# Kernel tuning notes

Hardware: AMD Instinct MI355X
Metric: run time of the kernel (lower is better)

The kernel has to match this reference:

```python
import jax, jax.numpy as jnp
import numpy as np

B = 131072   # batch of state samples
H = 512      # hidden width of reconstructed subnets
EPS_DIAG = 0.1  # diagonal regularization ensuring M is invertible


def setup_inputs() -> dict:
    key = jax.random.key(0)
    ks = jax.random.split(key, 20)
    f32 = jnp.float32
    inp = {
        "q":      jax.random.normal(ks[0], (B, 3), dtype=f32),
        "q_dot":  jax.random.normal(ks[1], (B, 3), dtype=f32),
        "s":      jax.random.normal(ks[2], (B, 3), dtype=f32),
        "s_Ddot": jax.random.normal(ks[3], (B, 3), dtype=f32),
        "tau":    jax.random.normal(ks[4], (B, 3), dtype=f32),
        # viscous / coulomb friction coefficients (f_v1..3, f_c1..3)
        "fv": jnp.full((3,), 0.05, dtype=f32),
        "fc": jnp.full((3,), 0.05, dtype=f32),
        # Mass net: 3 -> H -> 9
        "W1m": jax.random.normal(ks[5], (3, H), dtype=f32) * 0.1,
        "b1m": jnp.zeros((H,), dtype=f32),
        "W2m": jax.random.normal(ks[6], (H, 9), dtype=f32) * 0.05,
        "b2m": jnp.zeros((9,), dtype=f32),
        # Gravity net: 3 -> H -> 3
        "W1g": jax.random.normal(ks[7], (3, H), dtype=f32) * 0.1,
        "b1g": jnp.zeros((H,), dtype=f32),
        "W2g": jax.random.normal(ks[8], (H, 3), dtype=f32) * 0.05,
        "b2g": jnp.zeros((3,), dtype=f32),
        # KAB net: concat(q, s, s_Ddot)=9 -> H -> 3
        "W1k": jax.random.normal(ks[9], (9, H), dtype=f32) * 0.1,
        "b1k": jnp.zeros((H,), dtype=f32),
        "W2k": jax.random.normal(ks[10], (H, 3), dtype=f32) * 0.05,
        "b2k": jnp.zeros((3,), dtype=f32),
    }
    return inp


def reference(q, q_dot, s, s_Ddot, tau, fv, fc,
              W1m, b1m, W2m, b2m,
              W1g, b1g, W2g, b2g,
              W1k, b1k, W2k, b2k) -> jnp.ndarray:
    # Mass matrix net -> [B,3,3], made SPD-ish so inv(M) is well defined
    hm = jnp.tanh(q @ W1m + b1m)                       # [B,H]
    Mraw = (hm @ W2m + b2m).reshape(-1, 3, 3)          # [B,3,3]
    M = jnp.einsum('bij,bkj->bik', Mraw, Mraw) + EPS_DIAG * jnp.eye(3, dtype=q.dtype)

    # Gravity net -> [B,3]
    hg = jnp.tanh(q @ W1g + b1g)
    G = hg @ W2g + b2g

    # KAB net on concat(q, s, s_Ddot) -> [B,3]
    x = jnp.concatenate([q, s, s_Ddot], axis=-1)       # [B,9]
    hk = jnp.tanh(x @ W1k + b1k)
    KAB = hk @ W2k + b2k

    # diag(fv) @ q_dot and diag(fc) @ sign(q_dot) are elementwise scalings
    rhs = -G + KAB - fv * q_dot - fc * jnp.sign(q_dot) + tau  # [B,3]

    # q_Ddot = inv(M) @ rhs  (solve is the same math, fewer ops)
    q_Ddot = jnp.linalg.solve(M, rhs[..., None]).squeeze(-1)  # [B,3]
    return q_Ddot
```

## Files before the change

kernel.cpp:

```cpp
#include <hip/hip_runtime.h>
#include <math.h>

#define HDIM 512
#define NCH1 96
#define NCH2 48
#define EPS_DIAG 0.1f

typedef __fp16 h2 __attribute__((ext_vector_type(2)));
typedef __fp16 h8 __attribute__((ext_vector_type(8)));
typedef float f32x4 __attribute__((ext_vector_type(4)));
typedef unsigned int u32x4 __attribute__((ext_vector_type(4)));

__device__ __forceinline__ h2 f2h2(float a, float b) {
    return __builtin_amdgcn_cvt_pkrtz(a, b);
}

__device__ __forceinline__ h2 tanh2(h2 x) {
    const h2 HI = {(__fp16)2.0f,        (__fp16)2.0f};
    const h2 LO = {(__fp16)-2.0f,       (__fp16)-2.0f};
    const h2 C0 = {(__fp16)0.993654f,   (__fp16)0.993654f};
    const h2 C1 = {(__fp16)-0.29463f,   (__fp16)-0.29463f};
    const h2 C2 = {(__fp16)0.0695331f,  (__fp16)0.0695331f};
    const h2 C3 = {(__fp16)-0.00696328f,(__fp16)-0.00696328f};
    h2 t = __builtin_elementwise_min(__builtin_elementwise_max(x, LO), HI);
    h2 u = t * t;
    h2 p = __builtin_elementwise_fma(C3, u, C2);
    p = __builtin_elementwise_fma(p, u, C1);
    p = __builtin_elementwise_fma(p, u, C0);
    return t * p;
}

__device__ __forceinline__ float w1c_at(int k, int hid,
    const float* W1m, const float* b1m, const float* W1g, const float* b1g,
    const float* W1k, const float* b1k)
{
    if (hid < 512)  { if (k < 3) return W1m[k*HDIM + hid]; if (k == 9) return b1m[hid]; return 0.f; }
    if (hid < 1024) { const int h = hid - 512;
                      if (k < 3) return W1g[k*HDIM + h];  if (k == 9) return b1g[h];  return 0.f; }
    const int h = hid - 1024;
    if (k < 9) return W1k[k*HDIM + h]; if (k == 9) return b1k[h]; return 0.f;
}

__global__ void pack_frags(const float* __restrict__ W1m, const float* __restrict__ b1m,
                           const float* __restrict__ W2m,
                           const float* __restrict__ W1g, const float* __restrict__ b1g,
                           const float* __restrict__ W2g,
                           const float* __restrict__ W1k, const float* __restrict__ b1k,
                           const float* __restrict__ W2k,
                           __fp16* __restrict__ frag)
{
    const int tid = blockIdx.x * blockDim.x + threadIdx.x;
    if (tid >= (NCH1 + NCH2) * 64) return;
    const int c = tid >> 6, l = tid & 63;
    const int m = l & 15, kq = l >> 4;
    __fp16* dst = frag + (size_t)tid * 8;
    if (c < NCH1) {
        const int t = c >> 1, phase = c & 1;
        const int hid = 32*t + 8*(m >> 2) + (m & 3) + 4*phase;
        #pragma unroll
        for (int j = 0; j < 8; ++j) {
            const int k = kq*8 + j;
            dst[j] = (__fp16)((k < 10) ? w1c_at(k, hid, W1m, b1m, W1g, b1g, W1k, b1k) : 0.f);
        }
    } else {
        const int t = c - NCH1;
        #pragma unroll
        for (int j = 0; j < 8; ++j) {
            const int hid = 32*t + kq*8 + j;
            float v = 0.f;
            if (hid < 512)       { if (m < 9)             v = W2m[hid*9 + m]; }
            else if (hid < 1024) { if (m >= 9 && m < 12)  v = W2g[(hid-512)*3 + (m-9)]; }
            else                 { if (m >= 12 && m < 15) v = W2k[(hid-1024)*3 + (m-12)]; }
            dst[j] = (__fp16)v;
        }
    }
}

__global__ __launch_bounds__(256, 8) void dyn_kernel(
    const __fp16* __restrict__ frag,
    const float* __restrict__ q, const float* __restrict__ q_dot,
    const float* __restrict__ s, const float* __restrict__ s_Ddot,
    const float* __restrict__ tau,
    const float* __restrict__ fv, const float* __restrict__ fc,
    const float* __restrict__ b2m, const float* __restrict__ b2g,
    const float* __restrict__ b2k,
    float* __restrict__ out, int n)
{
    __shared__ float ebuf[4][16][20];

    const int lane = threadIdx.x & 63;
    const int w    = threadIdx.x >> 6;
    const int col  = lane & 15;
    const int quad = lane >> 4;
    const int base16 = (blockIdx.x * 4 + w) * 16;

    int sm = base16 + col; if (sm >= n) sm = n - 1;
    const float q0 = q[3*sm+0], q1 = q[3*sm+1], q2 = q[3*sm+2];
    const float s0 = s[3*sm+0], s1 = s[3*sm+1], s2 = s[3*sm+2];
    const float d0 = s_Ddot[3*sm+0], d1 = s_Ddot[3*sm+1], d2 = s_Ddot[3*sm+2];
    const bool z0 = (quad == 0), z1 = (quad == 1);
    h8 ax;
    ax[0] = (__fp16)(z0 ? q0 : (z1 ? d2  : 0.f));
    ax[1] = (__fp16)(z0 ? q1 : (z1 ? 1.f : 0.f));
    ax[2] = (__fp16)(z0 ? q2 : 0.f);
    ax[3] = (__fp16)(z0 ? s0 : 0.f);
    ax[4] = (__fp16)(z0 ? s1 : 0.f);
    ax[5] = (__fp16)(z0 ? s2 : 0.f);
    ax[6] = (__fp16)(z0 ? d0 : 0.f);
    ax[7] = (__fp16)(z0 ? d1 : 0.f);

    const f32x4 zero4 = {0.f, 0.f, 0.f, 0.f};
    f32x4 acc = zero4;

    const h8* p1 = (const h8*)frag + lane;
    const h8* p2 = (const h8*)frag + (size_t)NCH1 * 64 + lane;

#define BODY(W1A, W1B, W2V) do {                                              \
        f32x4 pa = __builtin_amdgcn_mfma_f32_16x16x32_f16((W1A), ax, zero4, 0, 0, 0); \
        f32x4 pb = __builtin_amdgcn_mfma_f32_16x16x32_f16((W1B), ax, zero4, 0, 0, 0); \
        const h2 A01 = tanh2(f2h2(pa[0], pa[1]));                             \
        const h2 A23 = tanh2(f2h2(pa[2], pa[3]));                             \
        const h2 B01 = tanh2(f2h2(pb[0], pb[1]));                             \
        const h2 B23 = tanh2(f2h2(pb[2], pb[3]));                             \
        u32x4 uv;                                                             \
        uv[0] = __builtin_bit_cast(unsigned int, A01);                        \
        uv[1] = __builtin_bit_cast(unsigned int, A23);                        \
        uv[2] = __builtin_bit_cast(unsigned int, B01);                        \
        uv[3] = __builtin_bit_cast(unsigned int, B23);                        \
        const h8 a2 = __builtin_bit_cast(h8, uv);                             \
        acc = __builtin_amdgcn_mfma_f32_16x16x32_f16((W2V), a2, acc, 0, 0, 0); \
    } while (0)

    h8 a0 = p1[0], b0 = p1[64], c0 = p2[0];
    int t = 0;
    for (; t < NCH2 - 2; t += 2) {
        h8 a1 = p1[128], b1 = p1[192], c1 = p2[64];
        p1 += 256; p2 += 128;
        BODY(a0, b0, c0);
        a0 = p1[0]; b0 = p1[64]; c0 = p2[0];
        BODY(a1, b1, c1);
    }
    {
        h8 a1 = p1[128], b1 = p1[192], c1 = p2[64];
        BODY(a0, b0, c0);
        BODY(a1, b1, c1);
    }
#undef BODY

    *(f32x4*)(&ebuf[w][col][4*quad]) = acc;
    asm volatile("s_waitcnt lgkmcnt(0)" ::: "memory");

    if (lane < 16) {
        const int i = base16 + lane;
        if (i < n) {
            const float* R = ebuf[w][lane];
            const float bM0 = R[0]  + b2m[0], bM1 = R[1]  + b2m[1], bM2 = R[2]  + b2m[2];
            const float bM3 = R[3]  + b2m[3], bM4 = R[4]  + b2m[4], bM5 = R[5]  + b2m[5];
            const float bM6 = R[6]  + b2m[6], bM7 = R[7]  + b2m[7], bM8 = R[8]  + b2m[8];
            const float bG0 = R[9]  + b2g[0], bG1 = R[10] + b2g[1], bG2 = R[11] + b2g[2];
            const float bK0 = R[12] + b2k[0], bK1 = R[13] + b2k[1], bK2 = R[14] + b2k[2];

            const float m00 = bM0*bM0 + bM1*bM1 + bM2*bM2 + EPS_DIAG;
            const float m01 = bM0*bM3 + bM1*bM4 + bM2*bM5;
            const float m02 = bM0*bM6 + bM1*bM7 + bM2*bM8;
            const float m11 = bM3*bM3 + bM4*bM4 + bM5*bM5 + EPS_DIAG;
            const float m12 = bM3*bM6 + bM4*bM7 + bM5*bM8;
            const float m22 = bM6*bM6 + bM7*bM7 + bM8*bM8 + EPS_DIAG;

            const float qd0 = q_dot[3*i+0], qd1 = q_dot[3*i+1], qd2 = q_dot[3*i+2];
            const float t0 = tau[3*i+0], t1 = tau[3*i+1], t2 = tau[3*i+2];
            const float fv0 = fv[0], fv1 = fv[1], fv2 = fv[2];
            const float fc0 = fc[0], fc1 = fc[1], fc2 = fc[2];
            const float sg0 = (qd0 > 0.f) ? 1.f : ((qd0 < 0.f) ? -1.f : 0.f);
            const float sg1 = (qd1 > 0.f) ? 1.f : ((qd1 < 0.f) ? -1.f : 0.f);
            const float sg2 = (qd2 > 0.f) ? 1.f : ((qd2 < 0.f) ? -1.f : 0.f);
            const float r0 = -bG0 + bK0 - fv0*qd0 - fc0*sg0 + t0;
            const float r1 = -bG1 + bK1 - fv1*qd1 - fc1*sg1 + t1;
            const float r2 = -bG2 + bK2 - fv2*qd2 - fc2*sg2 + t2;

            const float c00 = m11*m22 - m12*m12;
            const float c01 = m02*m12 - m01*m22;
            const float c02 = m01*m12 - m02*m11;
            const float det = m00*c00 + m01*c01 + m02*c02;
            const float idet = 1.0f / det;
            const float i11 = m00*m22 - m02*m02;
            const float i12 = m01*m02 - m00*m12;
            const float i22 = m00*m11 - m01*m01;

            out[3*i+0] = (c00*r0 + c01*r1 + c02*r2) * idet;
            out[3*i+1] = (c01*r0 + i11*r1 + i12*r2) * idet;
            out[3*i+2] = (c02*r0 + i12*r1 + i22*r2) * idet;
        }
    }
}

extern "C" void kernel_launch(void* const* d_in, const int* in_sizes, int n_in,
                              void* d_out, int out_size, void* d_ws, size_t ws_size,
                              hipStream_t stream) {
    const float* q      = (const float*)d_in[0];
    const float* q_dot  = (const float*)d_in[1];
    const float* s      = (const float*)d_in[2];
    const float* s_Ddot = (const float*)d_in[3];
    const float* tau    = (const float*)d_in[4];
    const float* fv     = (const float*)d_in[5];
    const float* fc     = (const float*)d_in[6];
    const float* W1m    = (const float*)d_in[7];
    const float* b1m    = (const float*)d_in[8];
    const float* W2m    = (const float*)d_in[9];
    const float* b2m    = (const float*)d_in[10];
    const float* W1g    = (const float*)d_in[11];
    const float* b1g    = (const float*)d_in[12];
    const float* W2g    = (const float*)d_in[13];
    const float* b2g    = (const float*)d_in[14];
    const float* W1k    = (const float*)d_in[15];
    const float* b1k    = (const float*)d_in[16];
    const float* W2k    = (const float*)d_in[17];
    const float* b2k    = (const float*)d_in[18];
    float* out = (float*)d_out;
    __fp16* frag = (__fp16*)d_ws;

    const int n = in_sizes[0] / 3;

    pack_frags<<<((NCH1 + NCH2) * 64 + 255) / 256, 256, 0, stream>>>(
        W1m, b1m, W2m, W1g, b1g, W2g, W1k, b1k, W2k, frag);

    const int blocks = (n + 63) / 64;
    dyn_kernel<<<blocks, 256, 0, stream>>>(frag, q, q_dot, s, s_Ddot, tau, fv, fc,
                                           b2m, b2g, b2k, out, n);
}
```

Baseline: 133.7 us.

## Process two 16-sample tiles per wave to reuse weight fragments

Each wave now handles 32 samples instead of 16, running two sets of MFMAs against each loaded weight fragment. This halves global/L2 weight fragment traffic per sample and halves the grid size, giving more independent MFMA work per loaded fragment. Launch bounds occupancy hint drops from 8 to 4 to allow more registers for the doubled accumulators and activations, which lowers occupancy. The epilogue now uses 32 lanes per wave for the solve.

```diff
diff --git a/kernel.cpp b/kernel.cpp
--- a/kernel.cpp
+++ b/kernel.cpp
@@ -76,7 +76,7 @@
     }
 }
 
-__global__ __launch_bounds__(256, 8) void dyn_kernel(
+__global__ __launch_bounds__(256, 4) void dyn_kernel(
     const __fp16* __restrict__ frag,
     const float* __restrict__ q, const float* __restrict__ q_dot,
     const float* __restrict__ s, const float* __restrict__ s_Ddot,
@@ -86,49 +86,68 @@
     const float* __restrict__ b2k,
     float* __restrict__ out, int n)
 {
-    __shared__ float ebuf[4][16][20];
+    __shared__ float ebuf[4][32][20];
 
     const int lane = threadIdx.x & 63;
     const int w    = threadIdx.x >> 6;
     const int col  = lane & 15;
     const int quad = lane >> 4;
-    const int base16 = (blockIdx.x * 4 + w) * 16;
-
-    int sm = base16 + col; if (sm >= n) sm = n - 1;
-    const float q0 = q[3*sm+0], q1 = q[3*sm+1], q2 = q[3*sm+2];
-    const float s0 = s[3*sm+0], s1 = s[3*sm+1], s2 = s[3*sm+2];
-    const float d0 = s_Ddot[3*sm+0], d1 = s_Ddot[3*sm+1], d2 = s_Ddot[3*sm+2];
-    const bool z0 = (quad == 0), z1 = (quad == 1);
-    h8 ax;
-    ax[0] = (__fp16)(z0 ? q0 : (z1 ? d2  : 0.f));
-    ax[1] = (__fp16)(z0 ? q1 : (z1 ? 1.f : 0.f));
-    ax[2] = (__fp16)(z0 ? q2 : 0.f);
-    ax[3] = (__fp16)(z0 ? s0 : 0.f);
-    ax[4] = (__fp16)(z0 ? s1 : 0.f);
-    ax[5] = (__fp16)(z0 ? s2 : 0.f);
-    ax[6] = (__fp16)(z0 ? d0 : 0.f);
-    ax[7] = (__fp16)(z0 ? d1 : 0.f);
+    const int base32 = (blockIdx.x * 4 + w) * 32;
+
+    h8 ax0, ax1;
+    {
+        int sm = base32 + col; if (sm >= n) sm = n - 1;
+        const float q0 = q[3*sm+0], q1 = q[3*sm+1], q2 = q[3*sm+2];
+        const float s0 = s[3*sm+0], s1 = s[3*sm+1], s2 = s[3*sm+2];
+        const float d0 = s_Ddot[3*sm+0], d1 = s_Ddot[3*sm+1], d2 = s_Ddot[3*sm+2];
+        const bool z0 = (quad == 0), z1 = (quad == 1);
+        ax0[0] = (__fp16)(z0 ? q0 : (z1 ? d2  : 0.f));
+        ax0[1] = (__fp16)(z0 ? q1 : (z1 ? 1.f : 0.f));
+        ax0[2] = (__fp16)(z0 ? q2 : 0.f);
+        ax0[3] = (__fp16)(z0 ? s0 : 0.f);
+        ax0[4] = (__fp16)(z0 ? s1 : 0.f);
+        ax0[5] = (__fp16)(z0 ? s2 : 0.f);
+        ax0[6] = (__fp16)(z0 ? d0 : 0.f);
+        ax0[7] = (__fp16)(z0 ? d1 : 0.f);
+    }
+    {
+        int sm = base32 + 16 + col; if (sm >= n) sm = n - 1;
+        const float q0 = q[3*sm+0], q1 = q[3*sm+1], q2 = q[3*sm+2];
+        const float s0 = s[3*sm+0], s1 = s[3*sm+1], s2 = s[3*sm+2];
+        const float d0 = s_Ddot[3*sm+0], d1 = s_Ddot[3*sm+1], d2 = s_Ddot[3*sm+2];
+        const bool z0 = (quad == 0), z1 = (quad == 1);
+        ax1[0] = (__fp16)(z0 ? q0 : (z1 ? d2  : 0.f));
+        ax1[1] = (__fp16)(z0 ? q1 : (z1 ? 1.f : 0.f));
+        ax1[2] = (__fp16)(z0 ? q2 : 0.f);
+        ax1[3] = (__fp16)(z0 ? s0 : 0.f);
+        ax1[4] = (__fp16)(z0 ? s1 : 0.f);
+        ax1[5] = (__fp16)(z0 ? s2 : 0.f);
+        ax1[6] = (__fp16)(z0 ? d0 : 0.f);
+        ax1[7] = (__fp16)(z0 ? d1 : 0.f);
+    }
 
     const f32x4 zero4 = {0.f, 0.f, 0.f, 0.f};
-    f32x4 acc = zero4;
+    f32x4 acc0 = zero4, acc1 = zero4;
 
     const h8* p1 = (const h8*)frag + lane;
     const h8* p2 = (const h8*)frag + (size_t)NCH1 * 64 + lane;
 
 #define BODY(W1A, W1B, W2V) do {                                              \
-        f32x4 pa = __builtin_amdgcn_mfma_f32_16x16x32_f16((W1A), ax, zero4, 0, 0, 0); \
-        f32x4 pb = __builtin_amdgcn_mfma_f32_16x16x32_f16((W1B), ax, zero4, 0, 0, 0); \
-        const h2 A01 = tanh2(f2h2(pa[0], pa[1]));                             \
-        const h2 A23 = tanh2(f2h2(pa[2], pa[3]));                             \
-        const h2 B01 = tanh2(f2h2(pb[0], pb[1]));                             \
-        const h2 B23 = tanh2(f2h2(pb[2], pb[3]));                             \
+        f32x4 pa0 = __builtin_amdgcn_mfma_f32_16x16x32_f16((W1A), ax0, zero4, 0, 0, 0); \
+        f32x4 pb0 = __builtin_amdgcn_mfma_f32_16x16x32_f16((W1B), ax0, zero4, 0, 0, 0); \
+        f32x4 pa1 = __builtin_amdgcn_mfma_f32_16x16x32_f16((W1A), ax1, zero4, 0, 0, 0); \
+        f32x4 pb1 = __builtin_amdgcn_mfma_f32_16x16x32_f16((W1B), ax1, zero4, 0, 0, 0); \
         u32x4 uv;                                                             \
-        uv[0] = __builtin_bit_cast(unsigned int, A01);                        \
-        uv[1] = __builtin_bit_cast(unsigned int, A23);                        \
-        uv[2] = __builtin_bit_cast(unsigned int, B01);                        \
-        uv[3] = __builtin_bit_cast(unsigned int, B23);                        \
-        const h8 a2 = __builtin_bit_cast(h8, uv);                             \
-        acc = __builtin_amdgcn_mfma_f32_16x16x32_f16((W2V), a2, acc, 0, 0, 0); \
+        uv[0] = __builtin_bit_cast(unsigned int, tanh2(f2h2(pa0[0], pa0[1]))); \
+        uv[1] = __builtin_bit_cast(unsigned int, tanh2(f2h2(pa0[2], pa0[3]))); \
+        uv[2] = __builtin_bit_cast(unsigned int, tanh2(f2h2(pb0[0], pb0[1]))); \
+        uv[3] = __builtin_bit_cast(unsigned int, tanh2(f2h2(pb0[2], pb0[3]))); \
+        acc0 = __builtin_amdgcn_mfma_f32_16x16x32_f16((W2V), __builtin_bit_cast(h8, uv), acc0, 0, 0, 0); \
+        uv[0] = __builtin_bit_cast(unsigned int, tanh2(f2h2(pa1[0], pa1[1]))); \
+        uv[1] = __builtin_bit_cast(unsigned int, tanh2(f2h2(pa1[2], pa1[3]))); \
+        uv[2] = __builtin_bit_cast(unsigned int, tanh2(f2h2(pb1[0], pb1[1]))); \
+        uv[3] = __builtin_bit_cast(unsigned int, tanh2(f2h2(pb1[2], pb1[3]))); \
+        acc1 = __builtin_amdgcn_mfma_f32_16x16x32_f16((W2V), __builtin_bit_cast(h8, uv), acc1, 0, 0, 0); \
     } while (0)
 
     h8 a0 = p1[0], b0 = p1[64], c0 = p2[0];
@@ -147,11 +166,12 @@
     }
 #undef BODY
 
-    *(f32x4*)(&ebuf[w][col][4*quad]) = acc;
+    *(f32x4*)(&ebuf[w][col][4*quad])      = acc0;
+    *(f32x4*)(&ebuf[w][16 + col][4*quad]) = acc1;
     asm volatile("s_waitcnt lgkmcnt(0)" ::: "memory");
 
-    if (lane < 16) {
-        const int i = base16 + lane;
+    if (lane < 32) {
+        const int i = base32 + lane;
         if (i < n) {
             const float* R = ebuf[w][lane];
             const float bM0 = R[0]  + b2m[0], bM1 = R[1]  + b2m[1], bM2 = R[2]  + b2m[2];
@@ -224,7 +244,7 @@
     pack_frags<<<((NCH1 + NCH2) * 64 + 255) / 256, 256, 0, stream>>>(
         W1m, b1m, W2m, W1g, b1g, W2g, W1k, b1k, W2k, frag);
 
-    const int blocks = (n + 63) / 64;
+    const int blocks = (n + 127) / 128;
     dyn_kernel<<<blocks, 256, 0, stream>>>(frag, q, q_dot, s, s_Ddot, tau, fv, fc,
                                            b2m, b2g, b2k, out, n);
 }
```

Result: faster. 129.3 us (-3.3%).

## Process four 16-sample tiles per wave to reuse weight fragments

Applied to the files above, without the earlier changes.

Each wave now handles 64 samples as four 16-sample MFMA tiles, with separate input fragments and accumulators per tile. Each weight fragment loaded from global memory is reused across all four tiles, cutting weight-load traffic per sample by four and giving the scheduler independent MFMA chains to interleave. The epilogue now uses all 64 lanes instead of 16. In exchange, register use rises (launch bounds relaxed from 8 to 2) and the grid shrinks fourfold, so fewer waves are resident per SIMD and latency hiding leans more on in-wave parallelism.

```diff
diff --git a/kernel.cpp b/kernel.cpp
--- a/kernel.cpp
+++ b/kernel.cpp
@@ -4,6 +4,7 @@
 #define HDIM 512
 #define NCH1 96
 #define NCH2 48
+#define NT   4
 #define EPS_DIAG 0.1f
 
 typedef __fp16 h2 __attribute__((ext_vector_type(2)));
@@ -76,7 +77,7 @@
     }
 }
 
-__global__ __launch_bounds__(256, 8) void dyn_kernel(
+__global__ __launch_bounds__(256, 2) void dyn_kernel(
     const __fp16* __restrict__ frag,
     const float* __restrict__ q, const float* __restrict__ q_dot,
     const float* __restrict__ s, const float* __restrict__ s_Ddot,
@@ -86,49 +87,52 @@
     const float* __restrict__ b2k,
     float* __restrict__ out, int n)
 {
-    __shared__ float ebuf[4][16][20];
+    __shared__ float ebuf[4][16 * NT][20];
 
     const int lane = threadIdx.x & 63;
     const int w    = threadIdx.x >> 6;
     const int col  = lane & 15;
     const int quad = lane >> 4;
-    const int base16 = (blockIdx.x * 4 + w) * 16;
-
-    int sm = base16 + col; if (sm >= n) sm = n - 1;
-    const float q0 = q[3*sm+0], q1 = q[3*sm+1], q2 = q[3*sm+2];
-    const float s0 = s[3*sm+0], s1 = s[3*sm+1], s2 = s[3*sm+2];
-    const float d0 = s_Ddot[3*sm+0], d1 = s_Ddot[3*sm+1], d2 = s_Ddot[3*sm+2];
-    const bool z0 = (quad == 0), z1 = (quad == 1);
-    h8 ax;
-    ax[0] = (__fp16)(z0 ? q0 : (z1 ? d2  : 0.f));
-    ax[1] = (__fp16)(z0 ? q1 : (z1 ? 1.f : 0.f));
-    ax[2] = (__fp16)(z0 ? q2 : 0.f);
-    ax[3] = (__fp16)(z0 ? s0 : 0.f);
-    ax[4] = (__fp16)(z0 ? s1 : 0.f);
-    ax[5] = (__fp16)(z0 ? s2 : 0.f);
-    ax[6] = (__fp16)(z0 ? d0 : 0.f);
-    ax[7] = (__fp16)(z0 ? d1 : 0.f);
+    const int baseS = (blockIdx.x * 4 + w) * (16 * NT);
+
+    h8 ax[NT];
+    #pragma unroll
+    for (int tt = 0; tt < NT; ++tt) {
+        int sm = baseS + tt*16 + col; if (sm >= n) sm = n - 1;
+        const float q0 = q[3*sm+0], q1 = q[3*sm+1], q2 = q[3*sm+2];
+        const float s0 = s[3*sm+0], s1 = s[3*sm+1], s2 = s[3*sm+2];
+        const float d0 = s_Ddot[3*sm+0], d1 = s_Ddot[3*sm+1], d2 = s_Ddot[3*sm+2];
+        const bool z0 = (quad == 0), z1 = (quad == 1);
+        ax[tt][0] = (__fp16)(z0 ? q0 : (z1 ? d2  : 0.f));
+        ax[tt][1] = (__fp16)(z0 ? q1 : (z1 ? 1.f : 0.f));
+        ax[tt][2] = (__fp16)(z0 ? q2 : 0.f);
+        ax[tt][3] = (__fp16)(z0 ? s0 : 0.f);
+        ax[tt][4] = (__fp16)(z0 ? s1 : 0.f);
+        ax[tt][5] = (__fp16)(z0 ? s2 : 0.f);
+        ax[tt][6] = (__fp16)(z0 ? d0 : 0.f);
+        ax[tt][7] = (__fp16)(z0 ? d1 : 0.f);
+    }
 
     const f32x4 zero4 = {0.f, 0.f, 0.f, 0.f};
-    f32x4 acc = zero4;
+    f32x4 acc[NT];
+    #pragma unroll
+    for (int tt = 0; tt < NT; ++tt) acc[tt] = zero4;
 
     const h8* p1 = (const h8*)frag + lane;
     const h8* p2 = (const h8*)frag + (size_t)NCH1 * 64 + lane;
 
 #define BODY(W1A, W1B, W2V) do {                                              \
-        f32x4 pa = __builtin_amdgcn_mfma_f32_16x16x32_f16((W1A), ax, zero4, 0, 0, 0); \
-        f32x4 pb = __builtin_amdgcn_mfma_f32_16x16x32_f16((W1B), ax, zero4, 0, 0, 0); \
-        const h2 A01 = tanh2(f2h2(pa[0], pa[1]));                             \
-        const h2 A23 = tanh2(f2h2(pa[2], pa[3]));                             \
-        const h2 B01 = tanh2(f2h2(pb[0], pb[1]));                             \
-        const h2 B23 = tanh2(f2h2(pb[2], pb[3]));                             \
-        u32x4 uv;                                                             \
-        uv[0] = __builtin_bit_cast(unsigned int, A01);                        \
-        uv[1] = __builtin_bit_cast(unsigned int, A23);                        \
-        uv[2] = __builtin_bit_cast(unsigned int, B01);                        \
-        uv[3] = __builtin_bit_cast(unsigned int, B23);                        \
-        const h8 a2 = __builtin_bit_cast(h8, uv);                             \
-        acc = __builtin_amdgcn_mfma_f32_16x16x32_f16((W2V), a2, acc, 0, 0, 0); \
+        _Pragma("unroll")                                                     \
+        for (int tt = 0; tt < NT; ++tt) {                                     \
+            f32x4 pa = __builtin_amdgcn_mfma_f32_16x16x32_f16((W1A), ax[tt], zero4, 0, 0, 0); \
+            f32x4 pb = __builtin_amdgcn_mfma_f32_16x16x32_f16((W1B), ax[tt], zero4, 0, 0, 0); \
+            u32x4 uv;                                                         \
+            uv[0] = __builtin_bit_cast(unsigned int, tanh2(f2h2(pa[0], pa[1]))); \
+            uv[1] = __builtin_bit_cast(unsigned int, tanh2(f2h2(pa[2], pa[3]))); \
+            uv[2] = __builtin_bit_cast(unsigned int, tanh2(f2h2(pb[0], pb[1]))); \
+            uv[3] = __builtin_bit_cast(unsigned int, tanh2(f2h2(pb[2], pb[3]))); \
+            acc[tt] = __builtin_amdgcn_mfma_f32_16x16x32_f16((W2V), __builtin_bit_cast(h8, uv), acc[tt], 0, 0, 0); \
+        }                                                                     \
     } while (0)
 
     h8 a0 = p1[0], b0 = p1[64], c0 = p2[0];
@@ -147,11 +151,13 @@
     }
 #undef BODY
 
-    *(f32x4*)(&ebuf[w][col][4*quad]) = acc;
+    #pragma unroll
+    for (int tt = 0; tt < NT; ++tt)
+        *(f32x4*)(&ebuf[w][tt*16 + col][4*quad]) = acc[tt];
     asm volatile("s_waitcnt lgkmcnt(0)" ::: "memory");
 
-    if (lane < 16) {
-        const int i = base16 + lane;
+    {
+        const int i = baseS + lane;
         if (i < n) {
             const float* R = ebuf[w][lane];
             const float bM0 = R[0]  + b2m[0], bM1 = R[1]  + b2m[1], bM2 = R[2]  + b2m[2];
@@ -224,7 +230,9 @@
     pack_frags<<<((NCH1 + NCH2) * 64 + 255) / 256, 256, 0, stream>>>(
         W1m, b1m, W2m, W1g, b1g, W2g, W1k, b1k, W2k, frag);
 
-    const int blocks = (n + 63) / 64;
-    dyn_kernel<<<blocks, 256, 0, stream>>>(frag, q, q_dot, s, s_Ddot, tau, fv, fc,
-                                           b2m, b2g, b2k, out, n);
-}
+    const int spb = 64 * NT * 4 / 4;
+    const int blocks = (n + 64*NT - 1) / (64*NT) / 1;
+    dyn_kernel<<<(n + 256 - 1) / 256, 256, 0, stream>>>(
+        frag, q, q_dot, s, s_Ddot, tau, fv, fc, b2m, b2g, b2k, out, n);
+    (void)spb; (void)blocks;
+}
```

Measured after the change: 133.2 us. Within noise of the previous version (-0.4%).
